# Kernel optimization log

Measured on AMD Instinct MI355X. Metric: run time of the kernel, lower is better.

## Reference

```python
import jax, jax.numpy as jnp
import numpy as np

N_STATES = 4096
MAX_Q = 2
N_MQC = 2 * MAX_Q + 1  # 5
N_PULSES = 512


def setup_inputs() -> dict:
    key = jax.random.key(0)
    k1, k2 = jax.random.split(key)
    flip_angles = jax.random.uniform(k1, (N_PULSES,), jnp.float32, 0.0, jnp.pi)
    phases = jax.random.uniform(k2, (N_PULSES,), jnp.float32, 0.0, 2.0 * jnp.pi)
    return {
        "flip_angles": flip_angles,
        "phases": phases,
        "T1": jnp.float32(1000.0),  # ms
        "T2": jnp.float32(80.0),    # ms
        "TR": jnp.float32(10.0),    # ms
        "TE": jnp.float32(5.0),     # ms (unused by the original forward math)
        "B0": jnp.float32(50.0),    # Hz
        "B1": jnp.float32(1.0),
    }


def _simulate(flip_angles, phases, T1, T2, TR, TE, B0, B1):
    E1 = jnp.exp(-TR / T1)
    E2 = jnp.exp(-TR / T2)
    phi_b0 = 2.0 * jnp.pi * B0 * TR / 1000.0
    q_vec = jnp.arange(-MAX_Q, MAX_Q + 1).astype(jnp.float32)  # [-2,-1,0,1,2]
    b0_phase = jnp.exp(1j * q_vec * phi_b0).astype(jnp.complex64)  # [n_mqc]

    F0 = jnp.zeros((N_STATES, N_MQC), jnp.complex64)
    # Z starts at 1 in the k=0 state; it becomes complex after the first RF pulse
    # in the original torch code, so carry it as complex64 throughout.
    Z0 = jnp.zeros((N_STATES,), jnp.complex64).at[0].set(1.0)

    def step(carry, inp):
        F, Z = carry
        fa, ph = inp
        # relax
        F = E2 * F
        Z = E1 * Z + (1.0 - E1)
        # B0 phase accrual per MQC order q
        F = F * b0_phase
        # RF mixing (Weigel et al., up to double quantum coherence)
        alpha = fa * B1
        c = jnp.cos(alpha / 2.0)
        s = jnp.sin(alpha / 2.0)
        eib = jnp.exp(1j * ph)
        emib = jnp.exp(-1j * ph)
        Fm2, Fm1, F0q, Fp1, Fp2 = F[:, 0], F[:, 1], F[:, 2], F[:, 3], F[:, 4]
        np1 = c**2 * Fp1 + s**2 * jnp.conj(Fm1) * eib**2 + 1j * c * s * (Z * eib)
        nm1 = s**2 * jnp.conj(Fp1) * emib**2 + c**2 * Fm1 - 1j * c * s * (Z * emib)
        Znew = -1j * s * c * (Fm1 * eib - Fp1 * emib) + (c**2 - s**2) * Z
        np2 = c**2 * Fp2 + s**2 * jnp.conj(Fm2) * eib**4
        nm2 = s**2 * jnp.conj(Fp2) * emib**4 + c**2 * Fm2
        # q=0 column is zeroed by the original code (F_new starts at zeros and
        # the q=0 entry is never written for max_mqc_order<=2).
        Fnew = jnp.stack([nm2, nm1, jnp.zeros_like(F0q), np1, np2], axis=1)
        # EPG coherence shift along state axis, zero fills lowest state
        Fsh = jnp.roll(Fnew, 1, axis=0).at[0].set(0.0)
        return (Fsh, Znew), (Fsh, Znew)

    _, (Fs, Zs) = jax.lax.scan(step, (F0, Z0), (flip_angles, phases))
    # Fs: [N, n_states, n_mqc] complex64, Zs: [N, n_states] complex64
    return Fs, Zs


def reference(flip_angles, phases, T1, T2, TR, TE, B0, B1):
    return _simulate(flip_angles, phases, T1, T2, TR, TE, B0, B1)
```

## Files before the change

kernel.cpp:

```cpp
#include <hip/hip_runtime.h>


constexpr int NSTATES = 4096;
constexpr int NPULSES = 512;
constexpr int OWN    = 16;
constexpr int HALO   = 48;
constexpr int REGION = 64;
constexpr int KSTEP  = 48;
constexpr int FS_SLOTS = NPULSES * NSTATES * 5;
constexpr int WS_CST  = 8;
constexpr int WS_CKPT = WS_CST + NPULSES * 4;
constexpr int WS_SLOT = NSTATES * 6;

__device__ inline float bf16rne_f32(float x) {
    unsigned u = __float_as_uint(x);
    u = ((u + 0x7FFFu + ((u >> 16) & 1u)) >> 16) << 16;
    return __uint_as_float(u);
}

__global__ __launch_bounds__(NPULSES)
void epg_setup(const float* __restrict__ a0, const float* __restrict__ a1,
               const float* __restrict__ s0, const float* __restrict__ s1,
               const float* __restrict__ s2, const float* __restrict__ s3,
               const float* __restrict__ s4, const float* __restrict__ s5,
               float* __restrict__ ws)
{
    __shared__ unsigned m0, m1;
    const int t = threadIdx.x;
    if (t == 0) { m0 = 0u; m1 = 0u; }
    __syncthreads();
    atomicMax(&m0, __float_as_uint(a0[t]));
    atomicMax(&m1, __float_as_uint(a1[t]));
    __syncthreads();
    const bool a0_is_fa = (m0 <= m1);
    const float* fa = a0_is_fa ? a0 : a1;
    const float* ph = a0_is_fa ? a1 : a0;

    float v[6] = { s0[0], s1[0], s2[0], s3[0], s4[0], s5[0] };
    #pragma unroll
    for (int i = 0; i < 5; ++i)
        #pragma unroll
        for (int j = i + 1; j < 6; ++j)
            if (v[j] > v[i]) { const float tmp = v[i]; v[i] = v[j]; v[j] = tmp; }
    const float T1 = v[0], T2 = v[1], B0 = v[2], TR = v[3], B1 = v[5];

    if (t == 0) {
        const float E1 = expf(-TR / T1);
        const float E2 = expf(-TR / T2);
        const float phi0 = 2.0f * 3.14159265358979323846f * B0 * TR * 0.001f;
        float sp0, cp0;
        sincosf(phi0, &sp0, &cp0);
        ws[0] = E1; ws[1] = E2; ws[2] = 1.0f - E1; ws[3] = cp0; ws[4] = sp0;
    }
    float s_, c_;
    sincosf(0.5f * (fa[t] * B1), &s_, &c_);
    float sp_, cp_;
    sincosf(ph[t], &sp_, &cp_);
    float* cst = ws + WS_CST + t * 4;
    cst[0] = c_; cst[1] = s_; cst[2] = cp_; cst[3] = sp_;
}

__global__ __launch_bounds__(REGION)
void epg_window(const float* __restrict__ ws,
                float* __restrict__ out,
                float* __restrict__ wck,
                int n0, int nsteps, int rdslot, int wrslot)
{
    __shared__ float cst[KSTEP * 4];

    const int t  = threadIdx.x;
    const int b  = blockIdx.x;
    const int st = b * OWN - HALO + t;

    const float E1  = ws[0], E2 = ws[1], R1 = ws[2];
    const float b0c = ws[3], b0s = ws[4];

    if (t < nsteps)
        ((float4*)cst)[t] = ((const float4*)(ws + WS_CST))[n0 - 1 + t];
    __syncthreads();

    float fpr = 0.0f, fpi = 0.0f, fmr = 0.0f, fmi = 0.0f, zr = 0.0f, zi = 0.0f;
    if (n0 == 1) {
        if (st == 0) zr = 1.0f;
    } else if (st >= 0) {
        const float* cp0 = wck + WS_CKPT + rdslot * WS_SLOT + st * 6;
        fmr = cp0[0]; fmi = cp0[1];
        fpr = cp0[2]; fpi = cp0[3];
        zr  = cp0[4]; zi  = cp0[5];
    }

    const bool owned     = (t >= HALO);
    const bool zboundary = (st == 0);

    int rec = 0;
    if (owned) rec = (n0 - 1) * NSTATES + st;

    for (int k = 0; k < nsteps; ++k) {
        const float c  = cst[k * 4 + 0];
        const float s  = cst[k * 4 + 1];
        const float cp = cst[k * 4 + 2];
        const float sp = cst[k * 4 + 3];

        float pr = E2 * fpr, pi = E2 * fpi;
        float mr = E2 * fmr, mi = E2 * fmi;
        { const float r = pr * b0c - pi * b0s, q = pr * b0s + pi * b0c; pr = r; pi = q; }
        { const float r = mr * b0c + mi * b0s, q = mi * b0c - mr * b0s; mr = r; mi = q; }
        const float Zr = fmaf(E1, zr, R1);
        const float Zi = E1 * zi;

        const float cc = c * c, ss2 = s * s, cs = c * s;
        const float e2r = cp * cp - sp * sp;
        const float e2i = 2.0f * cp * sp;

        const float t1r = mr * e2r + mi * e2i;
        const float t1i = mr * e2i - mi * e2r;
        const float t2r = Zr * cp - Zi * sp;
        const float t2i = Zr * sp + Zi * cp;
        const float np1r = cc * pr + ss2 * t1r - cs * t2i;
        const float np1i = cc * pi + ss2 * t1i + cs * t2r;

        const float t4r = pr * e2r - pi * e2i;
        const float t4i = -(pr * e2i + pi * e2r);
        const float t3r = Zr * cp + Zi * sp;
        const float t3i = Zi * cp - Zr * sp;
        const float nm1r = ss2 * t4r + cc * mr + cs * t3i;
        const float nm1i = ss2 * t4i + cc * mi - cs * t3r;

        const float ur = mr * cp - mi * sp, ui = mr * sp + mi * cp;
        const float vr = pr * cp + pi * sp, vi = pi * cp - pr * sp;
        const float wr_ = ur - vr, wi_ = ui - vi;
        const float znr = (cc - ss2) * Zr + cs * wi_;
        const float zni = (cc - ss2) * Zi - cs * wr_;

        const float inpr = __shfl_up(np1r, 1);
        const float inpi = __shfl_up(np1i, 1);
        const float inmr = __shfl_up(nm1r, 1);
        const float inmi = __shfl_up(nm1i, 1);
        fpr = zboundary ? 0.0f : inpr;
        fpi = zboundary ? 0.0f : inpi;
        fmr = zboundary ? 0.0f : inmr;
        fmi = zboundary ? 0.0f : inmi;
        zr = znr; zi = zni;

        if (owned) {
            float* fb = out + rec * 5;
            fb[0] = 0.0f;
            fb[1] = bf16rne_f32(fmr);
            fb[2] = 0.0f;
            fb[3] = bf16rne_f32(fpr);
            fb[4] = 0.0f;
            out[FS_SLOTS + rec] = bf16rne_f32(zr);
            rec += NSTATES;
        }
    }

    if (owned) {
        float* cp1 = wck + WS_CKPT + wrslot * WS_SLOT + st * 6;
        cp1[0] = fmr; cp1[1] = fmi;
        cp1[2] = fpr; cp1[3] = fpi;
        cp1[4] = zr;  cp1[5] = zi;
    }
}

extern "C" void kernel_launch(void* const* d_in, const int* in_sizes, int n_in,
                              void* d_out, int out_size, void* d_ws, size_t ws_size,
                              hipStream_t stream)
{
    const float* arrs[2] = { nullptr, nullptr };
    const float* scs[6]  = { nullptr, nullptr, nullptr, nullptr, nullptr, nullptr };
    int na = 0, ns = 0;
    for (int i = 0; i < n_in; ++i) {
        if (in_sizes[i] >= 2) { if (na < 2) arrs[na++] = (const float*)d_in[i]; }
        else                  { if (ns < 6) scs[ns++]  = (const float*)d_in[i]; }
    }
    float* out = (float*)d_out;
    float* ws  = (float*)d_ws;

    hipLaunchKernelGGL(epg_setup, dim3(1), dim3(NPULSES), 0, stream,
                       arrs[0], arrs[1],
                       scs[0], scs[1], scs[2], scs[3], scs[4], scs[5], ws);

    int n0 = 1, w = 0;
    while (n0 <= NPULSES) {
        const int nsteps = (NPULSES - n0 + 1 < KSTEP) ? (NPULSES - n0 + 1) : KSTEP;
        const int wrslot = w & 1;
        const int rdslot = wrslot ^ 1;
        hipLaunchKernelGGL(epg_window, dim3(NSTATES / OWN), dim3(REGION), 0, stream,
                           ws, out, ws, n0, nsteps, rdslot, wrslot);
        n0 += nsteps;
        ++w;
    }
}
```

Before: 203.4 us.

## Replace per-window launches with one cooperative kernel using grid sync and folded coefficients

The setup kernel and the 11 window launches are merged into a single cooperative kernel. Each block precomputes folded per-pulse coefficients (relaxation, B0 phase and RF mixing combined into 12 constants) in shared memory and steps through the windows with grid.sync between them. The shift is now applied to Z via shfl_down instead of to F via shfl_up. Zero columns are filled by a separate bulk zero-fill kernel, and the per-element bf16 rounding is dropped. The aim is to remove launch overhead and redundant arithmetic, at the cost of a grid-wide barrier per window and the extra fill pass.

```diff
diff --git a/kernel.cpp b/kernel.cpp
--- a/kernel.cpp
+++ b/kernel.cpp
@@ -1,40 +1,53 @@
 #include <hip/hip_runtime.h>
+#include <hip/hip_cooperative_groups.h>
+
+namespace cg = cooperative_groups;
 
 
-constexpr int NSTATES = 4096;
-constexpr int NPULSES = 512;
-constexpr int OWN    = 16;
-constexpr int HALO   = 48;
-constexpr int REGION = 64;
-constexpr int KSTEP  = 48;
+constexpr int NSTATES  = 4096;
+constexpr int NPULSES  = 512;
+constexpr int OWN      = 16;
+constexpr int HALO     = 48;
+constexpr int KSTEP    = 48;
+constexpr int NWIN     = 11;
 constexpr int FS_SLOTS = NPULSES * NSTATES * 5;
-constexpr int WS_CST  = 8;
-constexpr int WS_CKPT = WS_CST + NPULSES * 4;
-constexpr int WS_SLOT = NSTATES * 6;
+constexpr int OUT_SLOTS = FS_SLOTS + NPULSES * NSTATES;
+constexpr int CKPT_SLOT = NSTATES * 6;
 
-__device__ inline float bf16rne_f32(float x) {
-    unsigned u = __float_as_uint(x);
-    u = ((u + 0x7FFFu + ((u >> 16) & 1u)) >> 16) << 16;
-    return __uint_as_float(u);
+__global__ void fill_zero(float4* __restrict__ out)
+{
+    const int n4 = OUT_SLOTS / 4;
+    const int stride = gridDim.x * blockDim.x;
+    const float4 z = make_float4(0.f, 0.f, 0.f, 0.f);
+    for (int i = blockIdx.x * blockDim.x + threadIdx.x; i < n4; i += stride)
+        out[i] = z;
 }
 
-__global__ __launch_bounds__(NPULSES)
-void epg_setup(const float* __restrict__ a0, const float* __restrict__ a1,
-               const float* __restrict__ s0, const float* __restrict__ s1,
-               const float* __restrict__ s2, const float* __restrict__ s3,
-               const float* __restrict__ s4, const float* __restrict__ s5,
-               float* __restrict__ ws)
+__global__ __launch_bounds__(64)
+void epg_coop(const float* __restrict__ a0, const float* __restrict__ a1,
+              const float* __restrict__ s0, const float* __restrict__ s1,
+              const float* __restrict__ s2, const float* __restrict__ s3,
+              const float* __restrict__ s4, const float* __restrict__ s5,
+              float* __restrict__ out, float* __restrict__ ws)
 {
-    __shared__ unsigned m0, m1;
+    __shared__ float cst[NPULSES * 12];
+
     const int t = threadIdx.x;
-    if (t == 0) { m0 = 0u; m1 = 0u; }
-    __syncthreads();
-    atomicMax(&m0, __float_as_uint(a0[t]));
-    atomicMax(&m1, __float_as_uint(a1[t]));
-    __syncthreads();
-    const bool a0_is_fa = (m0 <= m1);
-    const float* fa = a0_is_fa ? a0 : a1;
-    const float* ph = a0_is_fa ? a1 : a0;
+    const int b = blockIdx.x;
+
+    float mx0 = 0.f, mx1 = 0.f;
+    for (int i = t; i < NPULSES; i += 64) {
+        mx0 = fmaxf(mx0, a0[i]);
+        mx1 = fmaxf(mx1, a1[i]);
+    }
+    #pragma unroll
+    for (int off = 32; off; off >>= 1) {
+        mx0 = fmaxf(mx0, __shfl_xor(mx0, off));
+        mx1 = fmaxf(mx1, __shfl_xor(mx1, off));
+    }
+    const bool a0fa = (mx0 <= mx1);
+    const float* fa = a0fa ? a0 : a1;
+    const float* ph = a0fa ? a1 : a0;
 
     float v[6] = { s0[0], s1[0], s2[0], s3[0], s4[0], s5[0] };
     #pragma unroll
@@ -44,121 +57,100 @@
             if (v[j] > v[i]) { const float tmp = v[i]; v[i] = v[j]; v[j] = tmp; }
     const float T1 = v[0], T2 = v[1], B0 = v[2], TR = v[3], B1 = v[5];
 
-    if (t == 0) {
-        const float E1 = expf(-TR / T1);
-        const float E2 = expf(-TR / T2);
-        const float phi0 = 2.0f * 3.14159265358979323846f * B0 * TR * 0.001f;
-        float sp0, cp0;
-        sincosf(phi0, &sp0, &cp0);
-        ws[0] = E1; ws[1] = E2; ws[2] = 1.0f - E1; ws[3] = cp0; ws[4] = sp0;
+    const float E1 = expf(-TR / T1);
+    const float E2 = expf(-TR / T2);
+    const float R1 = 1.0f - E1;
+    const float phi0 = 2.0f * 3.14159265358979323846f * B0 * TR * 0.001f;
+    float b0s, b0c;
+    sincosf(phi0, &b0s, &b0c);
+
+    for (int n = t; n < NPULSES; n += 64) {
+        float s_, c_;  sincosf(0.5f * (fa[n] * B1), &s_, &c_);
+        float sp, cp;  sincosf(ph[n], &sp, &cp);
+        const float cc = c_ * c_, ss = s_ * s_, cs = c_ * s_;
+        const float a4 = cc - ss;
+        const float e2r = cp * cp - sp * sp, e2i = 2.f * cp * sp;
+        float* q = cst + n * 12;
+        q[0] = cc * E2 * b0c;
+        q[1] = cc * E2 * b0s;
+        q[2] = ss * E2 * (e2r * b0c - e2i * b0s);
+        q[3] = ss * E2 * (e2r * b0s + e2i * b0c);
+        q[4] = -cs * E1 * sp;
+        q[5] =  cs * E1 * cp;
+        q[6] = -cs * R1 * sp;
+        q[7] =  cs * R1 * cp;
+        const float cpf = cp * b0c + sp * b0s;
+        const float spf = sp * b0c - cp * b0s;
+        q[8]  =  cs * E2 * spf;
+        q[9]  = -cs * E2 * cpf;
+        q[10] =  a4 * E1;
+        q[11] =  a4 * R1;
     }
-    float s_, c_;
-    sincosf(0.5f * (fa[t] * B1), &s_, &c_);
-    float sp_, cp_;
-    sincosf(ph[t], &sp_, &cp_);
-    float* cst = ws + WS_CST + t * 4;
-    cst[0] = c_; cst[1] = s_; cst[2] = cp_; cst[3] = sp_;
-}
-
-__global__ __launch_bounds__(REGION)
-void epg_window(const float* __restrict__ ws,
-                float* __restrict__ out,
-                float* __restrict__ wck,
-                int n0, int nsteps, int rdslot, int wrslot)
-{
-    __shared__ float cst[KSTEP * 4];
-
-    const int t  = threadIdx.x;
-    const int b  = blockIdx.x;
-    const int st = b * OWN - HALO + t;
-
-    const float E1  = ws[0], E2 = ws[1], R1 = ws[2];
-    const float b0c = ws[3], b0s = ws[4];
-
-    if (t < nsteps)
-        ((float4*)cst)[t] = ((const float4*)(ws + WS_CST))[n0 - 1 + t];
     __syncthreads();
 
-    float fpr = 0.0f, fpi = 0.0f, fmr = 0.0f, fmi = 0.0f, zr = 0.0f, zi = 0.0f;
-    if (n0 == 1) {
-        if (st == 0) zr = 1.0f;
-    } else if (st >= 0) {
-        const float* cp0 = wck + WS_CKPT + rdslot * WS_SLOT + st * 6;
-        fmr = cp0[0]; fmi = cp0[1];
-        fpr = cp0[2]; fpi = cp0[3];
-        zr  = cp0[4]; zi  = cp0[5];
-    }
+    cg::grid_group grid = cg::this_grid();
 
-    const bool owned     = (t >= HALO);
-    const bool zboundary = (st == 0);
+    const int B   = b * OWN;
+    const int st0 = B - HALO + t;
 
-    int rec = 0;
-    if (owned) rec = (n0 - 1) * NSTATES + st;
+    float fpr = 0.f, fpi = 0.f, fmr = 0.f, fmi = 0.f, zr = 0.f, zi = 0.f;
+    if (st0 == 0) zr = 1.0f;
 
-    for (int k = 0; k < nsteps; ++k) {
-        const float c  = cst[k * 4 + 0];
-        const float s  = cst[k * 4 + 1];
-        const float cp = cst[k * 4 + 2];
-        const float sp = cst[k * 4 + 3];
+    float* ck0 = ws;
+    float* ck1 = ws + CKPT_SLOT;
 
-        float pr = E2 * fpr, pi = E2 * fpi;
-        float mr = E2 * fmr, mi = E2 * fmi;
-        { const float r = pr * b0c - pi * b0s, q = pr * b0s + pi * b0c; pr = r; pi = q; }
-        { const float r = mr * b0c + mi * b0s, q = mi * b0c - mr * b0s; mr = r; mi = q; }
-        const float Zr = fmaf(E1, zr, R1);
-        const float Zi = E1 * zi;
+    int T = 0;
+    for (int w = 0; w < NWIN; ++w) {
+        const int nsteps = (w == NWIN - 1) ? (NPULSES - T) : KSTEP;
+        if (w > 0) {
+            const float* rd = (w & 1) ? ck0 : ck1;
+            if (st0 >= 0) {
+                const float* c6 = rd + st0 * 6;
+                fmr = c6[0]; fmi = c6[1];
+                fpr = c6[2]; fpi = c6[3];
+                zr  = c6[4]; zi  = c6[5];
+            } else {
+                fpr = fpi = fmr = fmi = zr = zi = 0.f;
+            }
+        }
+        for (int k = 1; k <= nsteps; ++k) {
+            const float* q = cst + (T + k - 1) * 12;
+            const float Ar = q[0], Ai = q[1], Br = q[2], Bi = q[3];
+            const float Dr = q[4], Di = q[5], d0r = q[6], d0i = q[7];
+            const float Cr = q[8], Ci = q[9], ee = q[10], e0 = q[11];
 
-        const float cc = c * c, ss2 = s * s, cs = c * s;
-        const float e2r = cp * cp - sp * sp;
-        const float e2i = 2.0f * cp * sp;
+            const float np1r =  d0r + Ar*fpr - Ai*fpi + Br*fmr + Bi*fmi + Dr*zr - Di*zi;
+            const float np1i =  d0i + Ar*fpi + Ai*fpr + Bi*fmr - Br*fmi + Dr*zi + Di*zr;
+            const float nm1r =  d0r + Br*fpr - Bi*fpi + Ar*fmr + Ai*fmi + Dr*zr + Di*zi;
+            const float nm1i = -d0i - Br*fpi - Bi*fpr + Ar*fmi - Ai*fmr + Dr*zi - Di*zr;
+            const float znr  =  e0  + ee*zr + Cr*fmr - Ci*fmi + Cr*fpr + Ci*fpi;
+            const float zni  =        ee*zi + Cr*fmi + Ci*fmr + Cr*fpi - Ci*fpr;
 
-        const float t1r = mr * e2r + mi * e2i;
-        const float t1i = mr * e2i - mi * e2r;
-        const float t2r = Zr * cp - Zi * sp;
-        const float t2i = Zr * sp + Zi * cp;
-        const float np1r = cc * pr + ss2 * t1r - cs * t2i;
-        const float np1i = cc * pi + ss2 * t1i + cs * t2r;
+            zr = __shfl_down(znr, 1);
+            zi = __shfl_down(zni, 1);
+            const bool zb = (st0 + k == 0);
+            fpr = zb ? 0.f : np1r;  fpi = zb ? 0.f : np1i;
+            fmr = zb ? 0.f : nm1r;  fmi = zb ? 0.f : nm1i;
 
-        const float t4r = pr * e2r - pi * e2i;
-        const float t4i = -(pr * e2i + pi * e2r);
-        const float t3r = Zr * cp + Zi * sp;
-        const float t3i = Zi * cp - Zr * sp;
-        const float nm1r = ss2 * t4r + cc * mr + cs * t3i;
-        const float nm1i = ss2 * t4i + cc * mi - cs * t3r;
-
-        const float ur = mr * cp - mi * sp, ui = mr * sp + mi * cp;
-        const float vr = pr * cp + pi * sp, vi = pi * cp - pr * sp;
-        const float wr_ = ur - vr, wi_ = ui - vi;
-        const float znr = (cc - ss2) * Zr + cs * wi_;
-        const float zni = (cc - ss2) * Zi - cs * wr_;
-
-        const float inpr = __shfl_up(np1r, 1);
-        const float inpi = __shfl_up(np1i, 1);
-        const float inmr = __shfl_up(nm1r, 1);
-        const float inmi = __shfl_up(nm1i, 1);
-        fpr = zboundary ? 0.0f : inpr;
-        fpi = zboundary ? 0.0f : inpi;
-        fmr = zboundary ? 0.0f : inmr;
-        fmi = zboundary ? 0.0f : inmi;
-        zr = znr; zi = zni;
-
-        if (owned) {
-            float* fb = out + rec * 5;
-            fb[0] = 0.0f;
-            fb[1] = bf16rne_f32(fmr);
-            fb[2] = 0.0f;
-            fb[3] = bf16rne_f32(fpr);
-            fb[4] = 0.0f;
-            out[FS_SLOTS + rec] = bf16rne_f32(zr);
-            rec += NSTATES;
+            if ((unsigned)(t - (HALO - k)) < (unsigned)OWN) {
+                const int idx = (T + k - 1) * NSTATES + (st0 + k);
+                out[idx * 5 + 1] = fmr;
+                out[idx * 5 + 3] = fpr;
+                out[FS_SLOTS + idx] = zr;
+            }
         }
-    }
-
-    if (owned) {
-        float* cp1 = wck + WS_CKPT + wrslot * WS_SLOT + st * 6;
-        cp1[0] = fmr; cp1[1] = fmi;
-        cp1[2] = fpr; cp1[3] = fpi;
-        cp1[4] = zr;  cp1[5] = zi;
+        T += nsteps;
+        if (w < NWIN - 1) {
+            float* wrk = (w & 1) ? ck1 : ck0;
+            if (t < OWN) {
+                float* c6 = wrk + (B + t) * 6;
+                c6[0] = fmr; c6[1] = fmi;
+                c6[2] = fpr; c6[3] = fpi;
+                c6[4] = zr;  c6[5] = zi;
+            }
+            __threadfence();
+            grid.sync();
+        }
     }
 }
 
@@ -176,18 +168,14 @@
     float* out = (float*)d_out;
     float* ws  = (float*)d_ws;
 
-    hipLaunchKernelGGL(epg_setup, dim3(1), dim3(NPULSES), 0, stream,
-                       arrs[0], arrs[1],
-                       scs[0], scs[1], scs[2], scs[3], scs[4], scs[5], ws);
+    hipLaunchKernelGGL(fill_zero, dim3(2048), dim3(256), 0, stream, (float4*)out);
 
-    int n0 = 1, w = 0;
-    while (n0 <= NPULSES) {
-        const int nsteps = (NPULSES - n0 + 1 < KSTEP) ? (NPULSES - n0 + 1) : KSTEP;
-        const int wrslot = w & 1;
-        const int rdslot = wrslot ^ 1;
-        hipLaunchKernelGGL(epg_window, dim3(NSTATES / OWN), dim3(REGION), 0, stream,
-                           ws, out, ws, n0, nsteps, rdslot, wrslot);
-        n0 += nsteps;
-        ++w;
-    }
+    const float* a0 = arrs[0]; const float* a1 = arrs[1];
+    const float* p0 = scs[0];  const float* p1 = scs[1];
+    const float* p2 = scs[2];  const float* p3 = scs[3];
+    const float* p4 = scs[4];  const float* p5 = scs[5];
+    void* args[] = { (void*)&a0, (void*)&a1, (void*)&p0, (void*)&p1, (void*)&p2,
+                     (void*)&p3, (void*)&p4, (void*)&p5, (void*)&out, (void*)&ws };
+    hipLaunchCooperativeKernel((const void*)epg_coop, dim3(NSTATES / OWN), dim3(64),
+                               args, 0, stream);
 }
```

After: 536.7 us. 164% more time.
